# Kernel tuning notes

Measured on AMD Instinct MI355X. Metric: run time of the kernel, lower is better.

## Reference

```python
import jax, jax.numpy as jnp
import numpy as np

N = 1024
ODE_UNFOLDS = 6
EPS = 1e-8
RICCATI_ITERS = 6  # fixed-point DARE iteration standing in for the (undefined) lqr() helper
MASK_DENSITY = 0.4


def lqr(A, B, Q, R):
    # Discrete-time Riccati iteration: P <- A'PA - A'PB (R+B'PB)^{-1} B'PA + Q
    P = Q
    for _ in range(RICCATI_ITERS):
        BtP = B.T @ P                         # [N,N]
        K = jnp.linalg.solve(R + BtP @ B, BtP @ A)
        P = A.T @ P @ (A - B @ K) + Q
    BtP = B.T @ P
    K = jnp.linalg.solve(R + BtP @ B, BtP @ A)
    return K, P


def setup_inputs() -> dict:
    key = jax.random.key(0)
    ks = jax.random.split(key, 24)
    u = lambda k, shape, lo, hi: jax.random.uniform(k, shape, jnp.float32, lo, hi)
    # sprandsym-style SPD laplacian param, rescaled to [0.001, 1]
    rng = np.random.default_rng(0)
    X = (rng.standard_normal((N, N)) * (rng.random((N, N)) < 0.1)).astype(np.float32)
    A = X @ X.T + 0.01 * np.eye(N, dtype=np.float32)
    A = (A - A.min()) / (A.max() - A.min())
    lap = (A * (1.0 - 0.001) + 0.001).astype(np.float32)

    mask = (jax.random.uniform(ks[2], (N, N)) < MASK_DENSITY).astype(jnp.float32)
    smask = (jax.random.uniform(ks[3], (N, N)) < MASK_DENSITY).astype(jnp.float32)
    return dict(
        inputs=jax.random.normal(ks[0], (N,), jnp.float32),
        adj=jax.random.uniform(ks[1], (N, N), jnp.float32) / N,  # scaled for numerical stability of the Riccati loop
        laplacian=jnp.asarray(lap),
        control=u(ks[6], (N,), 0.001, 4.0),
        gleak=u(ks[7], (N,), 0.001, 1.0),
        vleak=u(ks[8], (N,), -0.2, 0.2),
        cm=u(ks[9], (N,), 0.4, 0.6),
        sigma=u(ks[10], (N, N), 3.0, 8.0),
        mu=u(ks[11], (N, N), 0.3, 0.8),
        w=u(ks[12], (N, N), 0.001, 1.0),
        erev=jnp.sign(jax.random.normal(ks[4], (N, N))) * mask,
        sensory_sigma=u(ks[13], (N, N), 3.0, 8.0),
        sensory_mu=u(ks[14], (N, N), 0.3, 0.8),
        sensory_w=u(ks[15], (N, N), 0.001, 1.0),
        sensory_erev=jnp.sign(jax.random.normal(ks[5], (N, N))) * smask,
        sparsity_mask=mask,
        sensory_sparsity_mask=smask,
        input_w=jnp.ones((N,), jnp.float32),
        input_b=jnp.zeros((N,), jnp.float32),
        output_w=jnp.ones((N,), jnp.float32),
        output_b=jnp.zeros((N,), jnp.float32),
        attn_w=jax.random.normal(ks[16], (N,), jnp.float32) / jnp.sqrt(N),
        attn_b=jax.random.normal(ks[17], (1,), jnp.float32),
        gc_w=jax.random.normal(ks[18], (1, 1), jnp.float32),
        gc_b=jax.random.normal(ks[19], (1,), jnp.float32),
    )


def reference(inputs, adj, laplacian, control, gleak, vleak, cm, sigma, mu, w, erev,
              sensory_sigma, sensory_mu, sensory_w, sensory_erev,
              sparsity_mask, sensory_sparsity_mask,
              input_w, input_b, output_w, output_b, attn_w, attn_b, gc_w, gc_b):
    x = inputs * input_w + input_b                      # _map_inputs (affine)
    n = x.shape[0]

    # ControlAttention with R = Q = eye(N): fc(I) rows = attn_w + attn_b
    att = attn_w + attn_b[0]                            # [N]
    s = x * att
    att_e = jnp.exp(s - jnp.max(s))                     # stable exp weighting
    Qm = jnp.diag(att_e)
    Rm = jnp.diag(att_e)                                # Q_att == R_att since Q == R == I

    K, _ = lqr(adj, laplacian, Qm, Rm)                  # K: [N,N]
    ctrl = (control - jnp.mean(K * x, axis=1)) @ laplacian  # [N]

    # sensory synapse activation (constant over the unfold loop)
    sens_act = sensory_w * jax.nn.sigmoid(sensory_sigma * (x[:, None] - sensory_mu)) * sensory_sparsity_mask
    w_num_s = jnp.sum(sens_act * sensory_erev, axis=1)  # [N]
    w_den_s = jnp.sum(sens_act, axis=1)                 # [N]

    gcn = lambda h: jax.nn.relu(adj @ (h * gc_w[0, 0]) + gc_b[0])
    d = x[:, None]
    for _ in range(4):
        d = gcn(d)
    d = d[:, 0]

    cm_t = d + cm * ODE_UNFOLDS + ctrl                  # elapsed_time = 1.0 -> cm / (1/unfolds)

    v = jnp.zeros((n,), x.dtype)                        # states default: zeros
    for _ in range(ODE_UNFOLDS):
        w_act = w * jax.nn.sigmoid(sigma * (v[:, None] - mu)) * sparsity_mask
        w_num = jnp.sum(w_act * erev, axis=1) + w_num_s
        w_den = jnp.sum(w_act, axis=1) + w_den_s
        v = (cm_t * v + gleak * vleak + w_num) / (cm_t + gleak + w_den + EPS)

    out = v * output_w + output_b                       # motor_size == state_size path
    return out, v, laplacian, ctrl + control
```

## Files before the change

kernel.cpp:

```cpp
#include <hip/hip_runtime.h>

#define MSZ (1024*1024)
#define LD 1024
#define CFS_NB 128


__global__ __launch_bounds__(1024) void prep_k(const float* __restrict__ inp, const float* __restrict__ iw,
    const float* __restrict__ ib, const float* __restrict__ aw, const float* __restrict__ ab,
    float* __restrict__ xv, float* __restrict__ atte) {
  __shared__ float red[1024];
  int t = threadIdx.x;
  float x = inp[t] * iw[t] + ib[t];
  float s = x * (aw[t] + ab[0]);
  xv[t] = x;
  red[t] = s;
  __syncthreads();
  for (int o = 512; o > 0; o >>= 1) { if (t < o) red[t] = fmaxf(red[t], red[t + o]); __syncthreads(); }
  atte[t] = expf(s - red[0]);
}

__global__ void setdiag_k(float* __restrict__ P, const float* __restrict__ atte) {
  int idx = blockIdx.x * 256 + threadIdx.x;
  int r = idx >> 10, c = idx & 1023;
  P[idx] = (r == c) ? atte[r] : 0.0f;
}

__global__ __launch_bounds__(256) void sens_k(const float* __restrict__ sw, const float* __restrict__ ssig,
    const float* __restrict__ smu, const float* __restrict__ serev, const float* __restrict__ smask,
    const float* __restrict__ xv, float* __restrict__ wns, float* __restrict__ wds) {
  __shared__ float rn[256], rd[256];
  int i = blockIdx.x, t = threadIdx.x;
  float xi = xv[i];
  float n = 0.f, d = 0.f;
  for (int j = t; j < 1024; j += 256) {
    int idx = i * 1024 + j;
    float z = ssig[idx] * (xi - smu[idx]);
    float sg = 1.0f / (1.0f + expf(-z));
    float act = sw[idx] * sg * smask[idx];
    n += act * serev[idx];
    d += act;
  }
  rn[t] = n; rd[t] = d;
  __syncthreads();
  for (int o = 128; o > 0; o >>= 1) { if (t < o) { rn[t] += rn[t + o]; rd[t] += rd[t + o]; } __syncthreads(); }
  if (t == 0) { wns[i] = rn[0]; wds[i] = rd[0]; }
}

__global__ __launch_bounds__(256) void gcn_k(const float* __restrict__ adj, const float* __restrict__ hin,
    float* __restrict__ hout, const float* __restrict__ gcw, const float* __restrict__ gcb) {
  __shared__ float red[256];
  int i = blockIdx.x, t = threadIdx.x;
  float s = 0.f;
  for (int j = t; j < 1024; j += 256) s += adj[(size_t)i * 1024 + j] * hin[j];
  red[t] = s; __syncthreads();
  for (int o = 128; o > 0; o >>= 1) { if (t < o) red[t] += red[t + o]; __syncthreads(); }
  if (t == 0) hout[i] = fmaxf(gcw[0] * red[0] + gcb[0], 0.0f);
}

__global__ __launch_bounds__(256) void matvec_n_k(const float* __restrict__ M, const float* __restrict__ v,
    float* __restrict__ out) {
  __shared__ float red[256];
  int i = blockIdx.x, t = threadIdx.x;
  float s = 0.f;
  for (int j = t; j < 1024; j += 256) s += M[(size_t)i * 1024 + j] * v[j];
  red[t] = s; __syncthreads();
  for (int o = 128; o > 0; o >>= 1) { if (t < o) red[t] += red[t + o]; __syncthreads(); }
  if (t == 0) out[i] = red[0];
}

__global__ __launch_bounds__(256) void matvec_t_k(const float* __restrict__ M, const float* __restrict__ v,
    float* __restrict__ out) {
  int j = blockIdx.x * 256 + threadIdx.x;
  float s = 0.f;
  #pragma unroll 8
  for (int i = 0; i < 1024; i++) s += M[(size_t)i * 1024 + j] * v[i];
  out[j] = s;
}

__global__ void gctrl_k(const float* __restrict__ control, const float* __restrict__ u, float* __restrict__ g) {
  int t = blockIdx.x * 256 + threadIdx.x;
  g[t] = control[t] - u[t] * (1.0f / 1024.0f);
}

__global__ void copylap_k(const float4* __restrict__ src, float4* __restrict__ dst) {
  int i = blockIdx.x * 256 + threadIdx.x;
  dst[i] = src[i];
}


struct GDesc { const float* A; const float* B; float* C; const float* diag; int tri; int mode; };
struct GArgs { GDesc d[3]; };

template<int TA>
__global__ __launch_bounds__(256) void gemm64x128_k(GArgs ga) {
  GDesc de = ga.d[blockIdx.z];
  int row0 = blockIdx.y * 64, col0 = blockIdx.x * 128;
  if (de.tri && row0 + 64 <= col0) return;
  __shared__ float As[32][64];
  __shared__ float Bs[32][128];
  const float* __restrict__ A = de.A;
  const float* __restrict__ B = de.B;
  int t = threadIdx.x;
  int tx = t & 15, ty = t >> 4;
  float acc[4][8] = {};
  for (int k0 = 0; k0 < 1024; k0 += 32) {
    if (TA == 1) {
      #pragma unroll
      for (int h = 0; h < 2; h++) {
        int s = h * 256 + t;
        int bk = s >> 4, am = (s & 15) * 4;
        float4 v = *(const float4*)(A + (size_t)(k0 + bk) * LD + row0 + am);
        *(float4*)(&As[bk][am]) = v;
      }
    } else {
      #pragma unroll
      for (int h = 0; h < 2; h++) {
        int s = h * 256 + t;
        int am = s >> 3, k4 = (s & 7) * 4;
        float4 v = *(const float4*)(A + (size_t)(row0 + am) * LD + k0 + k4);
        As[k4 + 0][am] = v.x; As[k4 + 1][am] = v.y; As[k4 + 2][am] = v.z; As[k4 + 3][am] = v.w;
      }
    }
    #pragma unroll
    for (int h = 0; h < 4; h++) {
      int s = h * 256 + t;
      int bk = s >> 5, bn = (s & 31) * 4;
      float4 v = *(const float4*)(B + (size_t)(k0 + bk) * LD + col0 + bn);
      *(float4*)(&Bs[bk][bn]) = v;
    }
    __syncthreads();
    #pragma unroll
    for (int k = 0; k < 32; k++) {
      float4 a4 = *(float4*)(&As[k][tx * 4]);
      float4 b0 = *(float4*)(&Bs[k][ty * 8]);
      float4 b1 = *(float4*)(&Bs[k][ty * 8 + 4]);
      float a[4] = {a4.x, a4.y, a4.z, a4.w};
      float b[8] = {b0.x, b0.y, b0.z, b0.w, b1.x, b1.y, b1.z, b1.w};
      #pragma unroll
      for (int i = 0; i < 4; i++)
        #pragma unroll
        for (int j = 0; j < 8; j++)
          acc[i][j] += a[i] * b[j];
    }
    __syncthreads();
  }
  #pragma unroll
  for (int i = 0; i < 4; i++) {
    int gm = row0 + tx * 4 + i;
    if (de.diag) {
      int dc = gm - col0 - ty * 8;
      if (dc >= 0 && dc < 8) acc[i][dc] += de.diag[gm];
    }
    float* cp = de.C + (size_t)gm * LD + col0 + ty * 8;
    if (de.mode == 0) {
      float4 o0 = {acc[i][0], acc[i][1], acc[i][2], acc[i][3]};
      float4 o1 = {acc[i][4], acc[i][5], acc[i][6], acc[i][7]};
      *(float4*)cp = o0; *(float4*)(cp + 4) = o1;
    } else {
      float4 c0 = *(float4*)cp, c1 = *(float4*)(cp + 4);
      c0.x -= acc[i][0]; c0.y -= acc[i][1]; c0.z -= acc[i][2]; c0.w -= acc[i][3];
      c1.x -= acc[i][4]; c1.y -= acc[i][5]; c1.z -= acc[i][6]; c1.w -= acc[i][7];
      *(float4*)cp = c0; *(float4*)(cp + 4) = c1;
    }
  }
}


__device__ __forceinline__ void gsync(int* __restrict__ bar, int gen) {
  int t = threadIdx.x;
  int nb = gridDim.x;
  __syncthreads();
  if (blockIdx.x == 0) {
    if (t >= 1 && t < nb) {
      while (__hip_atomic_load(bar + t * 32, __ATOMIC_RELAXED, __HIP_MEMORY_SCOPE_AGENT) < gen)
        __builtin_amdgcn_s_sleep(2);
    }
    __syncthreads();
    if (t == 0) {
      __threadfence();
      __hip_atomic_store(bar + nb * 32, gen, __ATOMIC_RELAXED, __HIP_MEMORY_SCOPE_AGENT);
    }
    __syncthreads();
  } else {
    if (t == 0) {
      __threadfence();
      __hip_atomic_store(bar + blockIdx.x * 32, gen, __ATOMIC_RELAXED, __HIP_MEMORY_SCOPE_AGENT);
      while (__hip_atomic_load(bar + nb * 32, __ATOMIC_RELAXED, __HIP_MEMORY_SCOPE_AGENT) < gen)
        __builtin_amdgcn_s_sleep(8);
      __threadfence();
    }
    __syncthreads();
  }
}

__device__ __forceinline__ void potf2_lds(float (*T)[132], int l, float r[64]) {
  #pragma unroll
  for (int k = 0; k < 64; k++) r[k] = T[l][k];
  #pragma unroll
  for (int j = 0; j < 64; j++) {
    float dj = __shfl(r[j], j, 64);
    float Ljj = sqrtf(fmaxf(dj, 1e-12f));
    float inv = 1.0f / Ljj;
    if (l == j) r[j] = Ljj;
    else if (l > j) r[j] *= inv;
    #pragma unroll
    for (int k = j + 1; k < 64; k++) {
      float Lkj = __shfl(r[j], k, 64);
      r[k] -= r[j] * Lkj;
    }
  }
}

__global__ __launch_bounds__(256) void cfs_k(float* __restrict__ Mm, float* __restrict__ Lb,
                                             float* __restrict__ S, int* __restrict__ bar) {
  __shared__ float shA[64][68];
  __shared__ float shB[64][132];
  int t = threadIdx.x;
  int bid = blockIdx.x;
  int nb = gridDim.x;
  int gen = 0;

  if (bid == 0) {
    #pragma unroll
    for (int h = 0; h < 4; h++) {
      int q = h * 256 + t, r = q >> 4, c4 = (q & 15) * 4;
      *(float4*)(&shB[r][c4]) = *(const float4*)(Mm + (size_t)r * LD + c4);
    }
    __syncthreads();
    if (t < 64) {
      float r[64];
      potf2_lds(shB, t, r);
      #pragma unroll
      for (int k = 0; k < 64; k++) if (k <= t) Lb[(size_t)t * LD + k] = r[k];
    }
  }
  gsync(bar, ++gen);

  for (int s = 0; s < 16; s++) {
    int e = s * 64, e2 = e + 64, nt = 15 - s, rb = nt * 64;
    int nPanel = (rb + 255) / 256;
    int nRhs = S ? 4 : 0;
    int njA = nPanel + nRhs;
    if (bid < njA) {
      #pragma unroll
      for (int h = 0; h < 4; h++) {
        int q = h * 256 + t, r = q >> 4, c4 = (q & 15) * 4;
        *(float4*)(&shA[r][c4]) = *(const float4*)(Lb + (size_t)(e + r) * LD + e + c4);
      }
      __syncthreads();
      if (bid < nPanel) {
        int row = e2 + bid * 256 + t;
        if (row < 1024) {
          float y[64];
          #pragma unroll
          for (int k = 0; k < 64; k++) y[k] = Mm[(size_t)row * LD + e + k];
          #pragma unroll
          for (int kk = 0; kk < 64; kk++) {
            float v = y[kk];
            #pragma unroll
            for (int m = 0; m < kk; m++) v -= shA[kk][m] * y[m];
            y[kk] = v / shA[kk][kk];
          }
          #pragma unroll
          for (int k = 0; k < 64; k++) Lb[(size_t)row * LD + e + k] = y[k];
        }
      } else {
        int col = (bid - nPanel) * 256 + t;
        float y[64];
        #pragma unroll
        for (int k = 0; k < 64; k++) y[k] = S[(size_t)(e + k) * LD + col];
        #pragma unroll
        for (int kk = 0; kk < 64; kk++) {
          float v = y[kk];
          #pragma unroll
          for (int m = 0; m < kk; m++) v -= shA[kk][m] * y[m];
          y[kk] = v / shA[kk][kk];
        }
        #pragma unroll
        for (int k = 0; k < 64; k++) S[(size_t)(e + k) * LD + col] = y[k];
      }
    }
    gsync(bar, ++gen);
    if (nt > 0) {
      if (bid == 0) {
        #pragma unroll
        for (int h = 0; h < 4; h++) {
          int q = h * 256 + t, r = q >> 4, c4 = (q & 15) * 4;
          float4 v = *(const float4*)(Lb + (size_t)(e2 + r) * LD + e + c4);
          shA[c4 + 0][r] = v.x; shA[c4 + 1][r] = v.y; shA[c4 + 2][r] = v.z; shA[c4 + 3][r] = v.w;
          *(float4*)(&shB[r][c4]) = *(const float4*)(Mm + (size_t)(e2 + r) * LD + e2 + c4);
        }
        __syncthreads();
        {
          int tx = t & 15, ty = t >> 4;
          float acc[4][4] = {};
          #pragma unroll 8
          for (int k = 0; k < 64; k++) {
            float4 a4 = *(float4*)(&shA[k][tx * 4]);
            float4 b4 = *(float4*)(&shA[k][ty * 4]);
            float a[4] = {a4.x, a4.y, a4.z, a4.w};
            float b[4] = {b4.x, b4.y, b4.z, b4.w};
            #pragma unroll
            for (int i = 0; i < 4; i++)
              #pragma unroll
              for (int j = 0; j < 4; j++)
                acc[i][j] += a[i] * b[j];
          }
          #pragma unroll
          for (int i = 0; i < 4; i++)
            #pragma unroll
            for (int j = 0; j < 4; j++)
              shB[tx * 4 + i][ty * 4 + j] -= acc[i][j];
        }
        __syncthreads();
        if (t < 64) {
          float r[64];
          potf2_lds(shB, t, r);
          #pragma unroll
          for (int k = 0; k < 64; k++) if (k <= t) Lb[(size_t)(e2 + t) * LD + e2 + k] = r[k];
        }
      } else {
        int nSyrk = nt * (nt + 1) / 2 - 1;
        int nSupd = S ? nt * 8 : 0;
        int njB = nSyrk + nSupd;
        for (int job = bid - 1; job < njB; job += nb - 1) {
          if (job < nSyrk) {
            int q = job + 1;
            int i0 = (int)((sqrtf(8.0f * q + 1.0f) - 1.0f) * 0.5f);
            while ((i0 + 1) * (i0 + 2) / 2 <= q) i0++;
            while (i0 * (i0 + 1) / 2 > q) i0--;
            int j0 = q - i0 * (i0 + 1) / 2;
            int ra = e + 64 * (i0 + 1), rc = e + 64 * (j0 + 1);
            #pragma unroll
            for (int h = 0; h < 4; h++) {
              int qq = h * 256 + t, r = qq >> 4, c4 = (qq & 15) * 4;
              float4 v = *(const float4*)(Lb + (size_t)(ra + r) * LD + e + c4);
              shA[c4 + 0][r] = v.x; shA[c4 + 1][r] = v.y; shA[c4 + 2][r] = v.z; shA[c4 + 3][r] = v.w;
              float4 u = *(const float4*)(Lb + (size_t)(rc + r) * LD + e + c4);
              shB[c4 + 0][r] = u.x; shB[c4 + 1][r] = u.y; shB[c4 + 2][r] = u.z; shB[c4 + 3][r] = u.w;
            }
            __syncthreads();
            int tx = t & 15, ty = t >> 4;
            float acc[4][4] = {};
            #pragma unroll 8
            for (int k = 0; k < 64; k++) {
              float4 a4 = *(float4*)(&shA[k][tx * 4]);
              float4 b4 = *(float4*)(&shB[k][ty * 4]);
              float a[4] = {a4.x, a4.y, a4.z, a4.w};
              float b[4] = {b4.x, b4.y, b4.z, b4.w};
              #pragma unroll
              for (int i = 0; i < 4; i++)
                #pragma unroll
                for (int j = 0; j < 4; j++)
                  acc[i][j] += a[i] * b[j];
            }
            #pragma unroll
            for (int i = 0; i < 4; i++) {
              float* cp = Mm + (size_t)(ra + tx * 4 + i) * LD + rc + ty * 4;
              float4 c = *(float4*)cp;
              c.x -= acc[i][0]; c.y -= acc[i][1]; c.z -= acc[i][2]; c.w -= acc[i][3];
              *(float4*)cp = c;
            }
            __syncthreads();
          } else {
            int q = job - nSyrk;
            int i0 = (q >> 3) + 1, cb = q & 7;
            int ra = e + 64 * i0, c0 = cb * 128;
            #pragma unroll
            for (int h = 0; h < 4; h++) {
              int qq = h * 256 + t, r = qq >> 4, c4 = (qq & 15) * 4;
              float4 v = *(const float4*)(Lb + (size_t)(ra + r) * LD + e + c4);
              shA[c4 + 0][r] = v.x; shA[c4 + 1][r] = v.y; shA[c4 + 2][r] = v.z; shA[c4 + 3][r] = v.w;
            }
            #pragma unroll
            for (int h = 0; h < 8; h++) {
              int qq = h * 256 + t, r = qq >> 5, c4 = (qq & 31) * 4;
              *(float4*)(&shB[r][c4]) = *(const float4*)(S + (size_t)(e + r) * LD + c0 + c4);
            }
            __syncthreads();
            int tx = t & 15, ty = t >> 4;
            float acc[4][8] = {};
            #pragma unroll 8
            for (int k = 0; k < 64; k++) {
              float4 a4 = *(float4*)(&shA[k][tx * 4]);
              float4 b0 = *(float4*)(&shB[k][ty * 8]);
              float4 b1 = *(float4*)(&shB[k][ty * 8 + 4]);
              float a[4] = {a4.x, a4.y, a4.z, a4.w};
              float b[8] = {b0.x, b0.y, b0.z, b0.w, b1.x, b1.y, b1.z, b1.w};
              #pragma unroll
              for (int i = 0; i < 4; i++)
                #pragma unroll
                for (int j = 0; j < 8; j++)
                  acc[i][j] += a[i] * b[j];
            }
            #pragma unroll
            for (int i = 0; i < 4; i++) {
              float* cp = S + (size_t)(ra + tx * 4 + i) * LD + c0 + ty * 8;
              float4 v0 = *(float4*)cp, v1 = *(float4*)(cp + 4);
              v0.x -= acc[i][0]; v0.y -= acc[i][1]; v0.z -= acc[i][2]; v0.w -= acc[i][3];
              v1.x -= acc[i][4]; v1.y -= acc[i][5]; v1.z -= acc[i][6]; v1.w -= acc[i][7];
              *(float4*)cp = v0; *(float4*)(cp + 4) = v1;
            }
            __syncthreads();
          }
        }
      }
    }
    gsync(bar, ++gen);
  }
}

__global__ __launch_bounds__(256) void mirror_k(float* __restrict__ P, const float* __restrict__ atte) {
  __shared__ float tile[64][65];
  int b = blockIdx.x, t = threadIdx.x;
  int ti, tj;
  if (b < 16) { ti = b; tj = b; }
  else {
    int p = b - 16;
    ti = (int)((1.0f + sqrtf(1.0f + 8.0f * p)) * 0.5f);
    while (ti * (ti - 1) / 2 > p) ti--;
    while ((ti + 1) * ti / 2 <= p) ti++;
    tj = p - ti * (ti - 1) / 2;
  }
  #pragma unroll
  for (int h = 0; h < 4; h++) {
    int s = h * 256 + t;
    int r = s >> 4, c4 = (s & 15) * 4;
    *(float4*)(&tile[r][c4]) = *(const float4*)(P + (size_t)(ti * 64 + r) * LD + tj * 64 + c4);
  }
  __syncthreads();
  if (ti == tj) {
    #pragma unroll
    for (int h = 0; h < 4; h++) {
      int s = h * 256 + t;
      int r = s >> 4, c4 = (s & 15) * 4;
      #pragma unroll
      for (int j = 0; j < 4; j++) {
        int c = c4 + j;
        if (c > r) P[(size_t)(ti * 64 + r) * LD + tj * 64 + c] = tile[c][r];
        else if (c == r) P[(size_t)(ti * 64 + r) * LD + tj * 64 + c] = tile[r][r] + atte[ti * 64 + r];
      }
    }
  } else {
    #pragma unroll
    for (int h = 0; h < 4; h++) {
      int s = h * 256 + t;
      int r = s >> 4, c4 = (s & 15) * 4;
      float4 o = {tile[c4 + 0][r], tile[c4 + 1][r], tile[c4 + 2][r], tile[c4 + 3][r]};
      *(float4*)(P + (size_t)(tj * 64 + r) * LD + ti * 64 + c4) = o;
    }
  }
}


__global__ __launch_bounds__(1024) void trsv_fwd_k(const float* __restrict__ Lg, const float* __restrict__ bin,
    float* __restrict__ wout) {
  __shared__ float zs[1024];
  __shared__ float wsb[64];
  int t = threadIdx.x;
  zs[t] = bin[t];
  __syncthreads();
  for (int s = 0; s < 16; s++) {
    int e = s * 64;
    if (t < 64) {
      float rr[64];
      #pragma unroll
      for (int k = 0; k < 64; k++) rr[k] = Lg[(size_t)(e + t) * LD + e + k];
      float acc = zs[e + t];
      #pragma unroll
      for (int k = 0; k < 64; k++) {
        float cand = acc / rr[k];
        float wk = __shfl(cand, k, 64);
        if (t == k) wsb[k] = wk;
        if (t > k) acc -= rr[k] * wk;
      }
    }
    __syncthreads();
    if (t < 64) zs[e + t] = wsb[t];
    __syncthreads();
    if (t >= e + 64) {
      float a = zs[t];
      #pragma unroll
      for (int k = 0; k < 64; k++) a -= Lg[(size_t)t * LD + e + k] * wsb[k];
      zs[t] = a;
    }
    __syncthreads();
  }
  wout[t] = zs[t];
}

__global__ __launch_bounds__(1024) void trsv_bwd_k(const float* __restrict__ Lg, const float* __restrict__ bin,
    float* __restrict__ wout) {
  __shared__ float zs[1024];
  __shared__ float wsb[64];
  int t = threadIdx.x;
  zs[t] = bin[t];
  __syncthreads();
  for (int s = 15; s >= 0; s--) {
    int e = s * 64;
    if (t < 64) {
      float rr[64];
      #pragma unroll
      for (int k = 0; k < 64; k++) rr[k] = Lg[(size_t)(e + k) * LD + e + t];
      float acc = zs[e + t];
      #pragma unroll
      for (int k = 63; k >= 0; k--) {
        float cand = acc / rr[k];
        float wk = __shfl(cand, k, 64);
        if (t == k) wsb[k] = wk;
        if (t < k) acc -= rr[k] * wk;
      }
    }
    __syncthreads();
    if (t < 64) zs[e + t] = wsb[t];
    __syncthreads();
    if (t < e) {
      float a = zs[t];
      #pragma unroll
      for (int k = 0; k < 64; k++) a -= Lg[(size_t)(e + k) * LD + t] * wsb[k];
      zs[t] = a;
    }
    __syncthreads();
  }
  wout[t] = zs[t];
}

__global__ __launch_bounds__(256) void ode_k(const float* __restrict__ w, const float* __restrict__ sig,
    const float* __restrict__ mu, const float* __restrict__ erev, const float* __restrict__ mask,
    const float* __restrict__ gleak, const float* __restrict__ vleak, const float* __restrict__ cm,
    const float* __restrict__ dvec, const float* __restrict__ ctrlv, const float* __restrict__ wns,
    const float* __restrict__ wds, const float* __restrict__ ow, const float* __restrict__ ob,
    const float* __restrict__ control, float* __restrict__ dout) {
  __shared__ float wm[1024], we[1024], sgs[1024], mus[1024];
  __shared__ float red[512];
  __shared__ float vsh;
  int i = blockIdx.x, t = threadIdx.x;
  for (int j = t; j < 1024; j += 256) {
    int idx = i * 1024 + j;
    float wmv = w[idx] * mask[idx];
    wm[j] = wmv;
    we[j] = wmv * erev[idx];
    sgs[j] = sig[idx];
    mus[j] = mu[idx];
  }
  float cmt = dvec[i] + cm[i] * 6.0f + ctrlv[i];
  float gl = gleak[i], vl = vleak[i];
  float numS = wns[i], denS = wds[i];
  float v = 0.0f;
  __syncthreads();
  for (int u = 0; u < 6; u++) {
    float n = 0.f, d = 0.f;
    for (int j = t; j < 1024; j += 256) {
      float sgm = 1.0f / (1.0f + expf(-sgs[j] * (v - mus[j])));
      n += we[j] * sgm;
      d += wm[j] * sgm;
    }
    red[t] = n; red[256 + t] = d;
    __syncthreads();
    for (int o = 128; o > 0; o >>= 1) {
      if (t < o) { red[t] += red[t + o]; red[256 + t] += red[256 + t + o]; }
      __syncthreads();
    }
    if (t == 0) {
      float num = red[0] + numS, den = red[256] + denS;
      vsh = (cmt * v + gl * vl + num) / (cmt + gl + den + 1e-8f);
    }
    __syncthreads();
    v = vsh;
    __syncthreads();
  }
  if (t == 0) {
    dout[i] = v * ow[i] + ob[i];
    dout[1024 + i] = v;
    dout[2048 + 1048576 + i] = ctrlv[i] + control[i];
  }
}


extern "C" void kernel_launch(void* const* d_in, const int* in_sizes, int n_in,
                              void* d_out, int out_size, void* d_ws, size_t ws_size,
                              hipStream_t stream) {
  const float* inputs  = (const float*)d_in[0];
  const float* adj     = (const float*)d_in[1];
  const float* lap     = (const float*)d_in[2];
  const float* control = (const float*)d_in[3];
  const float* gleak   = (const float*)d_in[4];
  const float* vleak   = (const float*)d_in[5];
  const float* cm      = (const float*)d_in[6];
  const float* sigma   = (const float*)d_in[7];
  const float* mu      = (const float*)d_in[8];
  const float* w       = (const float*)d_in[9];
  const float* erev    = (const float*)d_in[10];
  const float* ssig    = (const float*)d_in[11];
  const float* smu     = (const float*)d_in[12];
  const float* sw      = (const float*)d_in[13];
  const float* serev   = (const float*)d_in[14];
  const float* mask    = (const float*)d_in[15];
  const float* smask   = (const float*)d_in[16];
  const float* iw      = (const float*)d_in[17];
  const float* ib      = (const float*)d_in[18];
  const float* ow      = (const float*)d_in[19];
  const float* ob      = (const float*)d_in[20];
  const float* aw      = (const float*)d_in[21];
  const float* ab      = (const float*)d_in[22];
  const float* gcw     = (const float*)d_in[23];
  const float* gcb     = (const float*)d_in[24];
  float* out = (float*)d_out;
  float* ws = (float*)d_ws;

  float* P0 = ws;
  float* P1 = ws + (size_t)MSZ;
  float* PA = ws + 2 * (size_t)MSZ;
  float* PB = ws + 3 * (size_t)MSZ;
  float* Mm = ws + 4 * (size_t)MSZ;
  float* S  = ws + 5 * (size_t)MSZ;
  float* vb = ws + 6 * (size_t)MSZ;
  float* xv = vb;            float* atte = vb + 1024;
  float* wns = vb + 2048;    float* wds  = vb + 3072;
  float* dA  = vb + 4096;    float* dB   = vb + 5120;
  float* yv  = vb + 6144;    float* tv   = vb + 7168;
  float* zv  = vb + 8192;    float* wv   = vb + 9216;
  float* uv  = vb + 10240;   float* gv   = vb + 11264;
  float* ctrlv = vb + 12288;
  int*   bar = (int*)(vb + 16384);

  const size_t barBytes = (size_t)(CFS_NB + 1) * 32 * sizeof(int);

  prep_k<<<1, 1024, 0, stream>>>(inputs, iw, ib, aw, ab, xv, atte);
  setdiag_k<<<4096, 256, 0, stream>>>(P0, atte);
  sens_k<<<1024, 256, 0, stream>>>(sw, ssig, smu, serev, smask, xv, wns, wds);
  gcn_k<<<1024, 256, 0, stream>>>(adj, xv, dA, gcw, gcb);
  gcn_k<<<1024, 256, 0, stream>>>(adj, dA, dB, gcw, gcb);
  gcn_k<<<1024, 256, 0, stream>>>(adj, dB, dA, gcw, gcb);
  gcn_k<<<1024, 256, 0, stream>>>(adj, dA, dB, gcw, gcb);

  float* P = P0; float* Pn = P1;
  for (int it = 0; it < 6; it++) {
    GArgs g1 = {{ {P, adj, PA, nullptr, 0, 0}, {P, lap, PB, nullptr, 0, 0}, {nullptr,nullptr,nullptr,nullptr,0,0} }};
    gemm64x128_k<0><<<dim3(8, 16, 2), 256, 0, stream>>>(g1);
    GArgs g2 = {{ {PB, adj, S, nullptr, 0, 0}, {PB, lap, Mm, atte, 1, 0}, {adj, PA, Pn, nullptr, 1, 0} }};
    gemm64x128_k<1><<<dim3(8, 16, 3), 256, 0, stream>>>(g2);
    hipMemsetAsync(bar, 0, barBytes, stream);
    cfs_k<<<CFS_NB, 256, 0, stream>>>(Mm, PA, S, bar);
    GArgs g3 = {{ {S, S, Pn, nullptr, 1, 1}, {nullptr,nullptr,nullptr,nullptr,0,0}, {nullptr,nullptr,nullptr,nullptr,0,0} }};
    gemm64x128_k<1><<<dim3(8, 16, 1), 256, 0, stream>>>(g3);
    mirror_k<<<136, 256, 0, stream>>>(Pn, atte);
    float* tmp = P; P = Pn; Pn = tmp;
  }

  GArgs g4 = {{ {P, lap, PB, nullptr, 0, 0}, {nullptr,nullptr,nullptr,nullptr,0,0}, {nullptr,nullptr,nullptr,nullptr,0,0} }};
  gemm64x128_k<0><<<dim3(8, 16, 1), 256, 0, stream>>>(g4);
  GArgs g5 = {{ {PB, lap, Mm, atte, 1, 0}, {nullptr,nullptr,nullptr,nullptr,0,0}, {nullptr,nullptr,nullptr,nullptr,0,0} }};
  gemm64x128_k<1><<<dim3(8, 16, 1), 256, 0, stream>>>(g5);
  hipMemsetAsync(bar, 0, barBytes, stream);
  cfs_k<<<CFS_NB, 256, 0, stream>>>(Mm, PA, nullptr, bar);
  matvec_n_k<<<1024, 256, 0, stream>>>(adj, xv, yv);
  matvec_n_k<<<1024, 256, 0, stream>>>(P, yv, tv);
  matvec_t_k<<<4, 256, 0, stream>>>(lap, tv, zv);
  trsv_fwd_k<<<1, 1024, 0, stream>>>(PA, zv, wv);
  trsv_bwd_k<<<1, 1024, 0, stream>>>(PA, wv, uv);
  gctrl_k<<<4, 256, 0, stream>>>(control, uv, gv);
  matvec_t_k<<<4, 256, 0, stream>>>(lap, gv, ctrlv);

  ode_k<<<1024, 256, 0, stream>>>(w, sigma, mu, erev, mask, gleak, vleak, cm, dB, ctrlv,
                                  wns, wds, ow, ob, control, out);
  copylap_k<<<1024, 256, 0, stream>>>((const float4*)lap, (float4*)(out + 2048));
}
```

Baseline: 16.35 ms.

## Redundantly factor diagonal block per block to halve grid barriers in Cholesky

Every block now factors the 64x64 diagonal block itself into a packed LDS triangle, and recomputes the panel TRSM rows it needs inside each SYRK and S-update job. This removes one of the two grid-wide barriers per step and the serial block-0 factor phase. Barrier buffers are preallocated per launch and zeroed once instead of a memset before each cfs launch, and the gsync fences are narrowed to release and acquire. The cost is redundant TRSM and POTF2 work in every block, plus a separate output buffer for the solved S.

```diff
diff --git a/kernel.cpp b/kernel.cpp
--- a/kernel.cpp
+++ b/kernel.cpp
@@ -3,6 +3,7 @@
 #define MSZ (1024*1024)
 #define LD 1024
 #define CFS_NB 128
+#define BAR_STRIDE (130*32)
 
 
 __global__ __launch_bounds__(1024) void prep_k(const float* __restrict__ inp, const float* __restrict__ iw,
@@ -177,17 +178,17 @@
     }
     __syncthreads();
     if (t == 0) {
-      __threadfence();
+      __builtin_amdgcn_fence(__ATOMIC_ACQ_REL, "agent");
       __hip_atomic_store(bar + nb * 32, gen, __ATOMIC_RELAXED, __HIP_MEMORY_SCOPE_AGENT);
     }
     __syncthreads();
   } else {
     if (t == 0) {
-      __threadfence();
+      __builtin_amdgcn_fence(__ATOMIC_RELEASE, "agent");
       __hip_atomic_store(bar + blockIdx.x * 32, gen, __ATOMIC_RELAXED, __HIP_MEMORY_SCOPE_AGENT);
       while (__hip_atomic_load(bar + nb * 32, __ATOMIC_RELAXED, __HIP_MEMORY_SCOPE_AGENT) < gen)
         __builtin_amdgcn_s_sleep(8);
-      __threadfence();
+      __builtin_amdgcn_fence(__ATOMIC_ACQUIRE, "agent");
     }
     __syncthreads();
   }
@@ -211,202 +212,168 @@
   }
 }
 
+__device__ __forceinline__ void trsm_row(const float* __restrict__ L11p, float y[64]) {
+  #pragma unroll
+  for (int kk = 0; kk < 64; kk++) {
+    float v = y[kk];
+    #pragma unroll
+    for (int m = 0; m < kk; m++) v -= L11p[kk * (kk + 1) / 2 + m] * y[m];
+    y[kk] = v / L11p[kk * (kk + 1) / 2 + kk];
+  }
+}
+
 __global__ __launch_bounds__(256) void cfs_k(float* __restrict__ Mm, float* __restrict__ Lb,
-                                             float* __restrict__ S, int* __restrict__ bar) {
+                                             float* __restrict__ S, float* __restrict__ Xb,
+                                             int* __restrict__ bar) {
+  __shared__ float L11p[2080];
   __shared__ float shA[64][68];
   __shared__ float shB[64][132];
-  int t = threadIdx.x;
-  int bid = blockIdx.x;
-  int nb = gridDim.x;
+  int t = threadIdx.x, bid = blockIdx.x, nb = gridDim.x;
   int gen = 0;
 
-  if (bid == 0) {
+  for (int s = 0; s < 16; s++) {
+    int e = s * 64, e2 = e + 64, nt = 15 - s, rb = nt * 64;
+
     #pragma unroll
     for (int h = 0; h < 4; h++) {
       int q = h * 256 + t, r = q >> 4, c4 = (q & 15) * 4;
-      *(float4*)(&shB[r][c4]) = *(const float4*)(Mm + (size_t)r * LD + c4);
+      *(float4*)(&shB[r][c4]) = *(const float4*)(Mm + (size_t)(e + r) * LD + e + c4);
     }
     __syncthreads();
     if (t < 64) {
       float r[64];
       potf2_lds(shB, t, r);
-      #pragma unroll
-      for (int k = 0; k < 64; k++) if (k <= t) Lb[(size_t)t * LD + k] = r[k];
-    }
-  }
-  gsync(bar, ++gen);
-
-  for (int s = 0; s < 16; s++) {
-    int e = s * 64, e2 = e + 64, nt = 15 - s, rb = nt * 64;
+      int base = t * (t + 1) / 2;
+      #pragma unroll
+      for (int k = 0; k < 64; k++) if (k <= t) L11p[base + k] = r[k];
+    }
+    __syncthreads();
+
     int nPanel = (rb + 255) / 256;
-    int nRhs = S ? 4 : 0;
-    int njA = nPanel + nRhs;
-    if (bid < njA) {
-      #pragma unroll
-      for (int h = 0; h < 4; h++) {
-        int q = h * 256 + t, r = q >> 4, c4 = (q & 15) * 4;
-        *(float4*)(&shA[r][c4]) = *(const float4*)(Lb + (size_t)(e + r) * LD + e + c4);
-      }
-      __syncthreads();
-      if (bid < nPanel) {
-        int row = e2 + bid * 256 + t;
+    int nSsol = S ? 4 : 0;
+    int nSyrk = nt * (nt + 1) / 2;
+    int nSupd = S ? nt * 8 : 0;
+    int base1 = 1, base2 = base1 + nPanel, base3 = base2 + nSsol, base4 = base3 + nSyrk;
+    int nJobs = base4 + nSupd;
+
+    for (int job = bid; job < nJobs; job += nb) {
+      if (job == 0) {
+        if (t < 64) {
+          int base = t * (t + 1) / 2;
+          #pragma unroll
+          for (int k = 0; k < 64; k++) if (k <= t) Lb[(size_t)(e + t) * LD + e + k] = L11p[base + k];
+        }
+      } else if (job < base2) {
+        int row = e2 + (job - base1) * 256 + t;
         if (row < 1024) {
           float y[64];
           #pragma unroll
           for (int k = 0; k < 64; k++) y[k] = Mm[(size_t)row * LD + e + k];
-          #pragma unroll
-          for (int kk = 0; kk < 64; kk++) {
-            float v = y[kk];
-            #pragma unroll
-            for (int m = 0; m < kk; m++) v -= shA[kk][m] * y[m];
-            y[kk] = v / shA[kk][kk];
-          }
+          trsm_row(L11p, y);
           #pragma unroll
           for (int k = 0; k < 64; k++) Lb[(size_t)row * LD + e + k] = y[k];
         }
-      } else {
-        int col = (bid - nPanel) * 256 + t;
+      } else if (job < base3) {
+        int col = (job - base2) * 256 + t;
         float y[64];
         #pragma unroll
         for (int k = 0; k < 64; k++) y[k] = S[(size_t)(e + k) * LD + col];
+        trsm_row(L11p, y);
         #pragma unroll
-        for (int kk = 0; kk < 64; kk++) {
-          float v = y[kk];
-          #pragma unroll
-          for (int m = 0; m < kk; m++) v -= shA[kk][m] * y[m];
-          y[kk] = v / shA[kk][kk];
-        }
-        #pragma unroll
-        for (int k = 0; k < 64; k++) S[(size_t)(e + k) * LD + col] = y[k];
-      }
-    }
-    gsync(bar, ++gen);
-    if (nt > 0) {
-      if (bid == 0) {
-        #pragma unroll
-        for (int h = 0; h < 4; h++) {
-          int q = h * 256 + t, r = q >> 4, c4 = (q & 15) * 4;
-          float4 v = *(const float4*)(Lb + (size_t)(e2 + r) * LD + e + c4);
-          shA[c4 + 0][r] = v.x; shA[c4 + 1][r] = v.y; shA[c4 + 2][r] = v.z; shA[c4 + 3][r] = v.w;
-          *(float4*)(&shB[r][c4]) = *(const float4*)(Mm + (size_t)(e2 + r) * LD + e2 + c4);
+        for (int k = 0; k < 64; k++) Xb[(size_t)(e + k) * LD + col] = y[k];
+      } else if (job < base4) {
+        int q = job - base3;
+        int i0 = (int)((sqrtf(8.0f * q + 1.0f) - 1.0f) * 0.5f);
+        while ((i0 + 1) * (i0 + 2) / 2 <= q) i0++;
+        while (i0 * (i0 + 1) / 2 > q) i0--;
+        int j0 = q - i0 * (i0 + 1) / 2;
+        int ra = e2 + i0 * 64, rc = e2 + j0 * 64;
+        if (t < 64) {
+          float y[64];
+          #pragma unroll
+          for (int k = 0; k < 64; k++) y[k] = Mm[(size_t)(ra + t) * LD + e + k];
+          trsm_row(L11p, y);
+          #pragma unroll
+          for (int k = 0; k < 64; k++) shA[k][t] = y[k];
+        } else if (t < 128) {
+          int r2 = t - 64;
+          float y[64];
+          #pragma unroll
+          for (int k = 0; k < 64; k++) y[k] = Mm[(size_t)(rc + r2) * LD + e + k];
+          trsm_row(L11p, y);
+          #pragma unroll
+          for (int k = 0; k < 64; k++) shB[k][r2] = y[k];
         }
         __syncthreads();
-        {
-          int tx = t & 15, ty = t >> 4;
-          float acc[4][4] = {};
-          #pragma unroll 8
-          for (int k = 0; k < 64; k++) {
-            float4 a4 = *(float4*)(&shA[k][tx * 4]);
-            float4 b4 = *(float4*)(&shA[k][ty * 4]);
-            float a[4] = {a4.x, a4.y, a4.z, a4.w};
-            float b[4] = {b4.x, b4.y, b4.z, b4.w};
-            #pragma unroll
-            for (int i = 0; i < 4; i++)
-              #pragma unroll
-              for (int j = 0; j < 4; j++)
-                acc[i][j] += a[i] * b[j];
-          }
+        int tx = t & 15, ty = t >> 4;
+        float acc[4][4] = {};
+        #pragma unroll 8
+        for (int k = 0; k < 64; k++) {
+          float4 a4 = *(float4*)(&shA[k][tx * 4]);
+          float4 b4 = *(float4*)(&shB[k][ty * 4]);
+          float a[4] = {a4.x, a4.y, a4.z, a4.w};
+          float b[4] = {b4.x, b4.y, b4.z, b4.w};
           #pragma unroll
           for (int i = 0; i < 4; i++)
             #pragma unroll
             for (int j = 0; j < 4; j++)
-              shB[tx * 4 + i][ty * 4 + j] -= acc[i][j];
+              acc[i][j] += a[i] * b[j];
+        }
+        #pragma unroll
+        for (int i = 0; i < 4; i++) {
+          float* cp = Mm + (size_t)(ra + tx * 4 + i) * LD + rc + ty * 4;
+          float4 c = *(float4*)cp;
+          c.x -= acc[i][0]; c.y -= acc[i][1]; c.z -= acc[i][2]; c.w -= acc[i][3];
+          *(float4*)cp = c;
         }
         __syncthreads();
+      } else {
+        int q = job - base4;
+        int ra = e2 + (q >> 3) * 64, c0 = (q & 7) * 128;
         if (t < 64) {
-          float r[64];
-          potf2_lds(shB, t, r);
-          #pragma unroll
-          for (int k = 0; k < 64; k++) if (k <= t) Lb[(size_t)(e2 + t) * LD + e2 + k] = r[k];
-        }
-      } else {
-        int nSyrk = nt * (nt + 1) / 2 - 1;
-        int nSupd = S ? nt * 8 : 0;
-        int njB = nSyrk + nSupd;
-        for (int job = bid - 1; job < njB; job += nb - 1) {
-          if (job < nSyrk) {
-            int q = job + 1;
-            int i0 = (int)((sqrtf(8.0f * q + 1.0f) - 1.0f) * 0.5f);
-            while ((i0 + 1) * (i0 + 2) / 2 <= q) i0++;
-            while (i0 * (i0 + 1) / 2 > q) i0--;
-            int j0 = q - i0 * (i0 + 1) / 2;
-            int ra = e + 64 * (i0 + 1), rc = e + 64 * (j0 + 1);
+          float y[64];
+          #pragma unroll
+          for (int k = 0; k < 64; k++) y[k] = Mm[(size_t)(ra + t) * LD + e + k];
+          trsm_row(L11p, y);
+          #pragma unroll
+          for (int k = 0; k < 64; k++) shA[k][t] = y[k];
+        } else if (t < 192) {
+          int c = c0 + (t - 64);
+          float y[64];
+          #pragma unroll
+          for (int k = 0; k < 64; k++) y[k] = S[(size_t)(e + k) * LD + c];
+          trsm_row(L11p, y);
+          #pragma unroll
+          for (int k = 0; k < 64; k++) shB[k][t - 64] = y[k];
+        }
+        __syncthreads();
+        int tx = t & 15, ty = t >> 4;
+        float acc[4][8] = {};
+        #pragma unroll 8
+        for (int k = 0; k < 64; k++) {
+          float4 a4 = *(float4*)(&shA[k][tx * 4]);
+          float4 b0 = *(float4*)(&shB[k][ty * 8]);
+          float4 b1 = *(float4*)(&shB[k][ty * 8 + 4]);
+          float a[4] = {a4.x, a4.y, a4.z, a4.w};
+          float b[8] = {b0.x, b0.y, b0.z, b0.w, b1.x, b1.y, b1.z, b1.w};
+          #pragma unroll
+          for (int i = 0; i < 4; i++)
             #pragma unroll
-            for (int h = 0; h < 4; h++) {
-              int qq = h * 256 + t, r = qq >> 4, c4 = (qq & 15) * 4;
-              float4 v = *(const float4*)(Lb + (size_t)(ra + r) * LD + e + c4);
-              shA[c4 + 0][r] = v.x; shA[c4 + 1][r] = v.y; shA[c4 + 2][r] = v.z; shA[c4 + 3][r] = v.w;
-              float4 u = *(const float4*)(Lb + (size_t)(rc + r) * LD + e + c4);
-              shB[c4 + 0][r] = u.x; shB[c4 + 1][r] = u.y; shB[c4 + 2][r] = u.z; shB[c4 + 3][r] = u.w;
-            }
-            __syncthreads();
-            int tx = t & 15, ty = t >> 4;
-            float acc[4][4] = {};
-            #pragma unroll 8
-            for (int k = 0; k < 64; k++) {
-              float4 a4 = *(float4*)(&shA[k][tx * 4]);
-              float4 b4 = *(float4*)(&shB[k][ty * 4]);
-              float a[4] = {a4.x, a4.y, a4.z, a4.w};
-              float b[4] = {b4.x, b4.y, b4.z, b4.w};
-              #pragma unroll
-              for (int i = 0; i < 4; i++)
-                #pragma unroll
-                for (int j = 0; j < 4; j++)
-                  acc[i][j] += a[i] * b[j];
-            }
-            #pragma unroll
-            for (int i = 0; i < 4; i++) {
-              float* cp = Mm + (size_t)(ra + tx * 4 + i) * LD + rc + ty * 4;
-              float4 c = *(float4*)cp;
-              c.x -= acc[i][0]; c.y -= acc[i][1]; c.z -= acc[i][2]; c.w -= acc[i][3];
-              *(float4*)cp = c;
-            }
-            __syncthreads();
-          } else {
-            int q = job - nSyrk;
-            int i0 = (q >> 3) + 1, cb = q & 7;
-            int ra = e + 64 * i0, c0 = cb * 128;
-            #pragma unroll
-            for (int h = 0; h < 4; h++) {
-              int qq = h * 256 + t, r = qq >> 4, c4 = (qq & 15) * 4;
-              float4 v = *(const float4*)(Lb + (size_t)(ra + r) * LD + e + c4);
-              shA[c4 + 0][r] = v.x; shA[c4 + 1][r] = v.y; shA[c4 + 2][r] = v.z; shA[c4 + 3][r] = v.w;
-            }
-            #pragma unroll
-            for (int h = 0; h < 8; h++) {
-              int qq = h * 256 + t, r = qq >> 5, c4 = (qq & 31) * 4;
-              *(float4*)(&shB[r][c4]) = *(const float4*)(S + (size_t)(e + r) * LD + c0 + c4);
-            }
-            __syncthreads();
-            int tx = t & 15, ty = t >> 4;
-            float acc[4][8] = {};
-            #pragma unroll 8
-            for (int k = 0; k < 64; k++) {
-              float4 a4 = *(float4*)(&shA[k][tx * 4]);
-              float4 b0 = *(float4*)(&shB[k][ty * 8]);
-              float4 b1 = *(float4*)(&shB[k][ty * 8 + 4]);
-              float a[4] = {a4.x, a4.y, a4.z, a4.w};
-              float b[8] = {b0.x, b0.y, b0.z, b0.w, b1.x, b1.y, b1.z, b1.w};
-              #pragma unroll
-              for (int i = 0; i < 4; i++)
-                #pragma unroll
-                for (int j = 0; j < 8; j++)
-                  acc[i][j] += a[i] * b[j];
-            }
-            #pragma unroll
-            for (int i = 0; i < 4; i++) {
-              float* cp = S + (size_t)(ra + tx * 4 + i) * LD + c0 + ty * 8;
-              float4 v0 = *(float4*)cp, v1 = *(float4*)(cp + 4);
-              v0.x -= acc[i][0]; v0.y -= acc[i][1]; v0.z -= acc[i][2]; v0.w -= acc[i][3];
-              v1.x -= acc[i][4]; v1.y -= acc[i][5]; v1.z -= acc[i][6]; v1.w -= acc[i][7];
-              *(float4*)cp = v0; *(float4*)(cp + 4) = v1;
-            }
-            __syncthreads();
-          }
-        }
+            for (int j = 0; j < 8; j++)
+              acc[i][j] += a[i] * b[j];
+        }
+        #pragma unroll
+        for (int i = 0; i < 4; i++) {
+          float* cp = S + (size_t)(ra + tx * 4 + i) * LD + c0 + ty * 8;
+          float4 v0 = *(float4*)cp, v1 = *(float4*)(cp + 4);
+          v0.x -= acc[i][0]; v0.y -= acc[i][1]; v0.z -= acc[i][2]; v0.w -= acc[i][3];
+          v1.x -= acc[i][4]; v1.y -= acc[i][5]; v1.z -= acc[i][6]; v1.w -= acc[i][7];
+          *(float4*)cp = v0; *(float4*)(cp + 4) = v1;
+        }
+        __syncthreads();
       }
     }
-    gsync(bar, ++gen);
+    if (s < 15) gsync(bar, ++gen);
   }
 }
 
@@ -622,9 +589,9 @@
   float* zv  = vb + 8192;    float* wv   = vb + 9216;
   float* uv  = vb + 10240;   float* gv   = vb + 11264;
   float* ctrlv = vb + 12288;
-  int*   bar = (int*)(vb + 16384);
-
-  const size_t barBytes = (size_t)(CFS_NB + 1) * 32 * sizeof(int);
+  int*   barBase = (int*)(vb + 16384);
+
+  hipMemsetAsync(barBase, 0, 7 * (size_t)BAR_STRIDE * sizeof(int), stream);
 
   prep_k<<<1, 1024, 0, stream>>>(inputs, iw, ib, aw, ab, xv, atte);
   setdiag_k<<<4096, 256, 0, stream>>>(P0, atte);
@@ -640,9 +607,8 @@
     gemm64x128_k<0><<<dim3(8, 16, 2), 256, 0, stream>>>(g1);
     GArgs g2 = {{ {PB, adj, S, nullptr, 0, 0}, {PB, lap, Mm, atte, 1, 0}, {adj, PA, Pn, nullptr, 1, 0} }};
     gemm64x128_k<1><<<dim3(8, 16, 3), 256, 0, stream>>>(g2);
-    hipMemsetAsync(bar, 0, barBytes, stream);
-    cfs_k<<<CFS_NB, 256, 0, stream>>>(Mm, PA, S, bar);
-    GArgs g3 = {{ {S, S, Pn, nullptr, 1, 1}, {nullptr,nullptr,nullptr,nullptr,0,0}, {nullptr,nullptr,nullptr,nullptr,0,0} }};
+    cfs_k<<<CFS_NB, 256, 0, stream>>>(Mm, PA, S, PB, barBase + it * BAR_STRIDE);
+    GArgs g3 = {{ {PB, PB, Pn, nullptr, 1, 1}, {nullptr,nullptr,nullptr,nullptr,0,0}, {nullptr,nullptr,nullptr,nullptr,0,0} }};
     gemm64x128_k<1><<<dim3(8, 16, 1), 256, 0, stream>>>(g3);
     mirror_k<<<136, 256, 0, stream>>>(Pn, atte);
     float* tmp = P; P = Pn; Pn = tmp;
@@ -652,8 +618,7 @@
   gemm64x128_k<0><<<dim3(8, 16, 1), 256, 0, stream>>>(g4);
   GArgs g5 = {{ {PB, lap, Mm, atte, 1, 0}, {nullptr,nullptr,nullptr,nullptr,0,0}, {nullptr,nullptr,nullptr,nullptr,0,0} }};
   gemm64x128_k<1><<<dim3(8, 16, 1), 256, 0, stream>>>(g5);
-  hipMemsetAsync(bar, 0, barBytes, stream);
-  cfs_k<<<CFS_NB, 256, 0, stream>>>(Mm, PA, nullptr, bar);
+  cfs_k<<<CFS_NB, 256, 0, stream>>>(Mm, PA, nullptr, PB, barBase + 6 * BAR_STRIDE);
   matvec_n_k<<<1024, 256, 0, stream>>>(adj, xv, yv);
   matvec_n_k<<<1024, 256, 0, stream>>>(P, yv, tv);
   matvec_t_k<<<4, 256, 0, stream>>>(lap, tv, zv);
```

New measurement: 29.43 ms. +80.0%, slower.
